# Optimization experiments

Measured on AMD Instinct MI355X. Metric: run time of the kernel, lower is better.

Reference implementation:

```python
import jax, jax.numpy as jnp
import numpy as np

N_NODES = 100000
N_EDGES = 3200000
IN_CH = 128
HID = 64
OUT_CH = 40


def setup_inputs() -> dict:
    key = jax.random.key(0)
    ks = jax.random.split(key, 12)
    x = jax.random.normal(ks[0], (N_NODES, IN_CH), dtype=jnp.float32)
    edge_index = jax.random.randint(ks[1], (2, N_EDGES), 0, N_NODES, dtype=jnp.int64)
    def lin(k, fan_in, fan_out):
        bound = 1.0 / np.sqrt(fan_in)
        kw, kb = jax.random.split(k)
        W = jax.random.uniform(kw, (fan_in, fan_out), minval=-bound, maxval=bound, dtype=jnp.float32)
        b = jax.random.uniform(kb, (fan_out,), minval=-bound, maxval=bound, dtype=jnp.float32)
        return W, b
    W1, b1 = lin(ks[2], IN_CH, HID)   # nn1 layer 1
    W2, b2 = lin(ks[3], HID, HID)     # nn1 layer 2
    W3, b3 = lin(ks[4], HID, HID)     # nn2 layer 1
    W4, b4 = lin(ks[5], HID, HID)     # nn2 layer 2
    Wf, bf = lin(ks[6], HID, OUT_CH)  # final fc
    return {"x": x, "edge_index": edge_index,
            "W1": W1, "b1": b1, "W2": W2, "b2": b2,
            "W3": W3, "b3": b3, "W4": W4, "b4": b4,
            "Wf": Wf, "bf": bf}


def _gin_conv(x, src, dst, W_a, b_a, W_b, b_b):
    # GINConv (eps=0): out = MLP(x + sum_{j->i} x_j)
    agg = jax.ops.segment_sum(x[src], dst, num_segments=x.shape[0])
    h = x + agg
    h = jax.nn.relu(h @ W_a + b_a)
    return h @ W_b + b_b


def reference(x, edge_index, W1, b1, W2, b2, W3, b3, W4, b4, Wf, bf):
    src, dst = edge_index[0], edge_index[1]
    h = _gin_conv(x, src, dst, W1, b1, W2, b2)
    h = jax.nn.relu(h)  # dropout is identity at eval
    h = _gin_conv(h, src, dst, W3, b3, W4, b4)
    h = jax.nn.relu(h)
    logits = h @ Wf + bf
    return jax.nn.log_softmax(logits, axis=1)
```

## Files before the change

kernel.cpp:

```cpp
#include <hip/hip_runtime.h>
#include <math.h>

#define N_NODES_C 100000
#define N_EDGES_C 3200000
#define NB 782
#define BNODES 128
#define LDS_CAP 6144
#define CHUNK 8192
#define NBLK 391

typedef unsigned short u16;

__device__ __forceinline__ float bf2f(u16 u) {
    unsigned int t = ((unsigned int)u) << 16;
    return __uint_as_float(t);
}
__device__ __forceinline__ u16 f2bf(float f) {
    unsigned int x = __float_as_uint(f);
    x += 0x7fffu + ((x >> 16) & 1u);
    return (u16)(x >> 16);
}


__global__ __launch_bounds__(256) void passA_hist_kernel(const int* __restrict__ dst,
                                                         int* __restrict__ cnt, int n_edges) {
    __shared__ int h[NB];
    for (int i = threadIdx.x; i < NB; i += 256) h[i] = 0;
    __syncthreads();
    const int blk = blockIdx.x;
    const int e0 = blk * CHUNK;
    const int cntE = min(CHUNK, n_edges - e0);
    for (int i = threadIdx.x * 4; i < cntE; i += 1024) {
        int4 d4 = *(const int4*)&dst[e0 + i];
        atomicAdd(&h[d4.x >> 7], 1); atomicAdd(&h[d4.y >> 7], 1);
        atomicAdd(&h[d4.z >> 7], 1); atomicAdd(&h[d4.w >> 7], 1);
    }
    __syncthreads();
    for (int i = threadIdx.x; i < NB; i += 256) cnt[i * NBLK + blk] = h[i];
}

__global__ __launch_bounds__(256) void scan_chunks_kernel(int* __restrict__ a, int n, int* __restrict__ bsums) {
    __shared__ int s[256];
    const int tid = threadIdx.x;
    int base = blockIdx.x * 1024 + tid * 4;
    int v[4];
#pragma unroll
    for (int i = 0; i < 4; ++i) v[i] = (base + i < n) ? a[base + i] : 0;
    int tsum = v[0] + v[1] + v[2] + v[3];
    s[tid] = tsum;
    __syncthreads();
    for (int off = 1; off < 256; off <<= 1) {
        int t = (tid >= off) ? s[tid - off] : 0;
        __syncthreads();
        s[tid] += t;
        __syncthreads();
    }
    int run = s[tid] - tsum;
#pragma unroll
    for (int i = 0; i < 4; ++i) {
        run += v[i];
        if (base + i < n) a[base + i] = run;
    }
    if (tid == 255) bsums[blockIdx.x] = s[255];
}

__global__ __launch_bounds__(512) void scan_sums_kernel(int* __restrict__ bsums, int nb) {
    __shared__ int s[512];
    const int tid = threadIdx.x;
    int v = (tid < nb) ? bsums[tid] : 0;
    s[tid] = v;
    __syncthreads();
    for (int off = 1; off < 512; off <<= 1) {
        int t = (tid >= off) ? s[tid - off] : 0;
        __syncthreads();
        s[tid] += t;
        __syncthreads();
    }
    if (tid < nb) bsums[tid] = s[tid] - v;
}

__global__ __launch_bounds__(256) void scan_add_kernel(int* __restrict__ a, int n, const int* __restrict__ bsums) {
    int base = blockIdx.x * 1024 + threadIdx.x * 4;
    int add = bsums[blockIdx.x];
#pragma unroll
    for (int i = 0; i < 4; ++i)
        if (base + i < n) a[base + i] += add;
}

__global__ __launch_bounds__(1024) void boffs_kernel(const int* __restrict__ incl,
                                                     int* __restrict__ boffs,
                                                     int* __restrict__ offs) {
    const int b = threadIdx.x;
    if (b < NB) boffs[b] = b ? incl[b * NBLK - 1] : 0;
    if (b == 0) {
        int total = incl[NB * NBLK - 1];
        boffs[NB] = total;
        offs[N_NODES_C] = total;
    }
}

__global__ __launch_bounds__(256) void passB_sort_kernel(const int* __restrict__ src,
                                                         const int* __restrict__ dst,
                                                         const int* __restrict__ incl,
                                                         unsigned int* __restrict__ stage,
                                                         int n_edges) {
    __shared__ unsigned int spack[CHUNK];
    __shared__ int hist[NB];
    __shared__ int lcur[NB];
    __shared__ int tsum[256];
    const int blk = blockIdx.x, tid = threadIdx.x;
    const int e0 = blk * CHUNK;
    const int cntE = min(CHUNK, n_edges - e0);

    for (int b = tid; b < NB; b += 256) hist[b] = 0;
    __syncthreads();

    for (int i = tid * 4; i < cntE; i += 1024) {
        int4 d4 = *(const int4*)&dst[e0 + i];
        atomicAdd(&hist[d4.x >> 7], 1); atomicAdd(&hist[d4.y >> 7], 1);
        atomicAdd(&hist[d4.z >> 7], 1); atomicAdd(&hist[d4.w >> 7], 1);
    }
    __syncthreads();

    {
        int loc[4];
        const int bi = tid * 4;
        int s = 0;
#pragma unroll
        for (int k = 0; k < 4; ++k) {
            int idx = bi + k;
            loc[k] = (idx < NB) ? hist[idx] : 0;
            s += loc[k];
        }
        tsum[tid] = s;
        __syncthreads();
        for (int off = 1; off < 256; off <<= 1) {
            int t = (tid >= off) ? tsum[tid - off] : 0;
            __syncthreads();
            tsum[tid] += t;
            __syncthreads();
        }
        int run = tsum[tid] - s;
#pragma unroll
        for (int k = 0; k < 4; ++k) {
            int idx = bi + k;
            if (idx < NB) {
                int h = loc[k];
                hist[idx] = run;
                lcur[idx] = run;
                run += h;
            }
        }
    }
    __syncthreads();

    for (int i = tid * 4; i < cntE; i += 1024) {
        int4 d4 = *(const int4*)&dst[e0 + i];
        int4 s4 = *(const int4*)&src[e0 + i];
        int p;
        p = atomicAdd(&lcur[d4.x >> 7], 1); spack[p] = (unsigned)s4.x | (((unsigned)d4.x & 127u) << 17);
        p = atomicAdd(&lcur[d4.y >> 7], 1); spack[p] = (unsigned)s4.y | (((unsigned)d4.y & 127u) << 17);
        p = atomicAdd(&lcur[d4.z >> 7], 1); spack[p] = (unsigned)s4.z | (((unsigned)d4.z & 127u) << 17);
        p = atomicAdd(&lcur[d4.w >> 7], 1); spack[p] = (unsigned)s4.w | (((unsigned)d4.w & 127u) << 17);
    }
    __syncthreads();

    for (int b = tid; b < NB; b += 256) {
        int l0 = hist[b];
        int l1 = (b + 1 < NB) ? hist[b + 1] : cntE;
        int idx = b * NBLK + blk;
        int g0 = idx ? incl[idx - 1] : 0;
        for (int j = l0; j < l1; ++j) stage[g0 + (j - l0)] = spack[j];
    }
}

__global__ __launch_bounds__(256) void bucket_finalize_kernel(const unsigned int* __restrict__ stage,
                                                              const int* __restrict__ boffs,
                                                              int* __restrict__ offs,
                                                              int* __restrict__ srcs) {
    __shared__ int hist[BNODES];
    __shared__ int excl[BNODES];
    __shared__ int curs[BNODES];
    __shared__ int sbuf[LDS_CAP];
    const int b = blockIdx.x, tid = threadIdx.x;
    const int base = boffs[b];
    const int count = boffs[b + 1] - base;
    const int n0 = b * BNODES;
    for (int i = tid; i < BNODES; i += 256) hist[i] = 0;
    __syncthreads();
    for (int i = tid; i < count; i += 256) {
        unsigned int w = stage[base + i];
        atomicAdd(&hist[w >> 17], 1);
    }
    __syncthreads();
    if (tid < BNODES) excl[tid] = hist[tid];
    __syncthreads();
    for (int off = 1; off < BNODES; off <<= 1) {
        int t = 0;
        if (tid < BNODES && tid >= off) t = excl[tid - off];
        __syncthreads();
        if (tid < BNODES) excl[tid] += t;
        __syncthreads();
    }
    if (tid < BNODES) {
        int ex = excl[tid] - hist[tid];
        int n = n0 + tid;
        if (n < N_NODES_C) offs[n] = base + ex;
        curs[tid] = ex;
    }
    __syncthreads();
    if (count <= LDS_CAP) {
        for (int i = tid; i < count; i += 256) {
            unsigned int w = stage[base + i];
            int p = atomicAdd(&curs[w >> 17], 1);
            sbuf[p] = (int)(w & 0x1FFFFu);
        }
        __syncthreads();
        for (int i = tid; i < count; i += 256) srcs[base + i] = sbuf[i];
    } else {
        for (int i = tid; i < count; i += 256) {
            unsigned int w = stage[base + i];
            int p = atomicAdd(&curs[w >> 17], 1);
            srcs[base + p] = (int)(w & 0x1FFFFu);
        }
    }
}


__global__ __launch_bounds__(256) void gather64v_kernel(const u16* __restrict__ feat,
                                                        const int* __restrict__ offs,
                                                        const int* __restrict__ srcs,
                                                        const float* __restrict__ bias,
                                                        u16* __restrict__ out, int n_nodes) {
    const int wave = threadIdx.x >> 6;
    const int lane = threadIdx.x & 63;
    const int grp  = lane >> 4;
    const int cl   = lane & 15;
    const int n = blockIdx.x * 4 + wave;
    if (n >= n_nodes) return;

    float a0 = 0.f, a1 = 0.f, a2 = 0.f, a3 = 0.f;
    if (grp == 0) {
        ushort4 v = *(const ushort4*)&feat[(size_t)n * 64 + cl * 4];
        a0 = bf2f(v.x); a1 = bf2f(v.y); a2 = bf2f(v.z); a3 = bf2f(v.w);
    }
    const int s0 = offs[n], s1 = offs[n + 1];
    int i = s0;
    for (; i + 32 <= s1; i += 32) {
        int r[8];
#pragma unroll
        for (int u = 0; u < 8; ++u) r[u] = srcs[i + u * 4 + grp];
        ushort4 v[8];
#pragma unroll
        for (int u = 0; u < 8; ++u) v[u] = *(const ushort4*)&feat[(size_t)r[u] * 64 + cl * 4];
#pragma unroll
        for (int u = 0; u < 8; ++u) {
            a0 += bf2f(v[u].x); a1 += bf2f(v[u].y); a2 += bf2f(v[u].z); a3 += bf2f(v[u].w);
        }
    }
    for (; i + 8 <= s1; i += 8) {
        int ra = srcs[i + grp];
        int rb = srcs[i + 4 + grp];
        ushort4 va = *(const ushort4*)&feat[(size_t)ra * 64 + cl * 4];
        ushort4 vb = *(const ushort4*)&feat[(size_t)rb * 64 + cl * 4];
        a0 += bf2f(va.x); a1 += bf2f(va.y); a2 += bf2f(va.z); a3 += bf2f(va.w);
        a0 += bf2f(vb.x); a1 += bf2f(vb.y); a2 += bf2f(vb.z); a3 += bf2f(vb.w);
    }
    for (; i + 4 <= s1; i += 4) {
        int rr = srcs[i + grp];
        ushort4 v = *(const ushort4*)&feat[(size_t)rr * 64 + cl * 4];
        a0 += bf2f(v.x); a1 += bf2f(v.y); a2 += bf2f(v.z); a3 += bf2f(v.w);
    }
    if (i + grp < s1) {
        int rr = srcs[i + grp];
        ushort4 v = *(const ushort4*)&feat[(size_t)rr * 64 + cl * 4];
        a0 += bf2f(v.x); a1 += bf2f(v.y); a2 += bf2f(v.z); a3 += bf2f(v.w);
    }
    a0 += __shfl_xor(a0, 16); a1 += __shfl_xor(a1, 16);
    a2 += __shfl_xor(a2, 16); a3 += __shfl_xor(a3, 16);
    a0 += __shfl_xor(a0, 32); a1 += __shfl_xor(a1, 32);
    a2 += __shfl_xor(a2, 32); a3 += __shfl_xor(a3, 32);
    if (lane < 16) {
        float4 b = *(const float4*)&bias[cl * 4];
        ushort4 o;
        o.x = f2bf(fmaxf(a0 + b.x, 0.f));
        o.y = f2bf(fmaxf(a1 + b.y, 0.f));
        o.z = f2bf(fmaxf(a2 + b.z, 0.f));
        o.w = f2bf(fmaxf(a3 + b.w, 0.f));
        *(ushort4*)&out[(size_t)n * 64 + cl * 4] = o;
    }
}

#define GIN_STEP(ai, i)                                                                               \
    acc[i][0] += ai.x * w0.x; acc[i][1] += ai.x * w0.y; acc[i][2] += ai.x * w0.z; acc[i][3] += ai.x * w0.w; \
    acc[i][0] += ai.y * w1.x; acc[i][1] += ai.y * w1.y; acc[i][2] += ai.y * w1.z; acc[i][3] += ai.y * w1.w; \
    acc[i][0] += ai.z * w2.x; acc[i][1] += ai.z * w2.y; acc[i][2] += ai.z * w2.z; acc[i][3] += ai.z * w2.w; \
    acc[i][0] += ai.w * w3.x; acc[i][1] += ai.w * w3.y; acc[i][2] += ai.w * w3.z; acc[i][3] += ai.w * w3.w;

#define BF4_TO_F4(u4) make_float4(bf2f(u4.x), bf2f(u4.y), bf2f(u4.z), bf2f(u4.w))


__global__ __launch_bounds__(256) void dense128_kernel(const float* __restrict__ in,
                                                       const float* __restrict__ W,
                                                       u16* __restrict__ out, int n_nodes) {
    __shared__ float sW[128 * 64];
    const int tid = threadIdx.x;
    for (int i = tid; i < 128 * 16; i += 256) ((float4*)sW)[i] = ((const float4*)W)[i];
    __syncthreads();
    const int tj = tid & 15, tn = tid >> 4;
    const int j0 = tj * 4, n0 = blockIdx.x * 64 + tn * 4;
    const int r0 = min(n0 + 0, n_nodes - 1), r1 = min(n0 + 1, n_nodes - 1);
    const int r2 = min(n0 + 2, n_nodes - 1), r3 = min(n0 + 3, n_nodes - 1);
    float acc[4][4];
#pragma unroll
    for (int i = 0; i < 4; ++i)
#pragma unroll
        for (int j = 0; j < 4; ++j) acc[i][j] = 0.f;
#pragma unroll 4
    for (int k = 0; k < 128; k += 4) {
        float4 a0 = *(const float4*)&in[(size_t)r0 * 128 + k];
        float4 a1 = *(const float4*)&in[(size_t)r1 * 128 + k];
        float4 a2 = *(const float4*)&in[(size_t)r2 * 128 + k];
        float4 a3 = *(const float4*)&in[(size_t)r3 * 128 + k];
        float4 w0 = *(const float4*)&sW[(k + 0) * 64 + j0];
        float4 w1 = *(const float4*)&sW[(k + 1) * 64 + j0];
        float4 w2 = *(const float4*)&sW[(k + 2) * 64 + j0];
        float4 w3 = *(const float4*)&sW[(k + 3) * 64 + j0];
        GIN_STEP(a0, 0) GIN_STEP(a1, 1) GIN_STEP(a2, 2) GIN_STEP(a3, 3)
    }
#pragma unroll
    for (int i = 0; i < 4; ++i) {
        int n = n0 + i;
        if (n < n_nodes) {
            ushort4 o;
            o.x = f2bf(acc[i][0]); o.y = f2bf(acc[i][1]);
            o.z = f2bf(acc[i][2]); o.w = f2bf(acc[i][3]);
            *(ushort4*)&out[(size_t)n * 64 + j0] = o;
        }
    }
}


__global__ __launch_bounds__(256) void fused_w2w3_kernel(const u16* __restrict__ in,
                                                         const float* __restrict__ W2,
                                                         const float* __restrict__ b2,
                                                         const float* __restrict__ W3,
                                                         u16* __restrict__ out, int n_nodes) {
    __shared__ float sW2[64 * 64];
    __shared__ float sW3[64 * 64];
    __shared__ float sT[64][68];
    const int tid = threadIdx.x;
    for (int i = tid; i < 64 * 16; i += 256) {
        ((float4*)sW2)[i] = ((const float4*)W2)[i];
        ((float4*)sW3)[i] = ((const float4*)W3)[i];
    }
    __syncthreads();
    const int tj = tid & 15, tn = tid >> 4;
    const int j0 = tj * 4, n0l = tn * 4;
    const int base = blockIdx.x * 64;
    const int r0 = min(base + n0l + 0, n_nodes - 1), r1 = min(base + n0l + 1, n_nodes - 1);
    const int r2 = min(base + n0l + 2, n_nodes - 1), r3 = min(base + n0l + 3, n_nodes - 1);
    float acc[4][4];
#pragma unroll
    for (int i = 0; i < 4; ++i)
#pragma unroll
        for (int j = 0; j < 4; ++j) acc[i][j] = b2[j0 + j];
#pragma unroll 4
    for (int k = 0; k < 64; k += 4) {
        ushort4 u0 = *(const ushort4*)&in[(size_t)r0 * 64 + k];
        ushort4 u1 = *(const ushort4*)&in[(size_t)r1 * 64 + k];
        ushort4 u2 = *(const ushort4*)&in[(size_t)r2 * 64 + k];
        ushort4 u3 = *(const ushort4*)&in[(size_t)r3 * 64 + k];
        float4 a0 = BF4_TO_F4(u0);
        float4 a1 = BF4_TO_F4(u1);
        float4 a2 = BF4_TO_F4(u2);
        float4 a3 = BF4_TO_F4(u3);
        float4 w0 = *(const float4*)&sW2[(k + 0) * 64 + j0];
        float4 w1 = *(const float4*)&sW2[(k + 1) * 64 + j0];
        float4 w2 = *(const float4*)&sW2[(k + 2) * 64 + j0];
        float4 w3 = *(const float4*)&sW2[(k + 3) * 64 + j0];
        GIN_STEP(a0, 0) GIN_STEP(a1, 1) GIN_STEP(a2, 2) GIN_STEP(a3, 3)
    }
#pragma unroll
    for (int i = 0; i < 4; ++i) {
        float4 t;
        t.x = fmaxf(acc[i][0], 0.f); t.y = fmaxf(acc[i][1], 0.f);
        t.z = fmaxf(acc[i][2], 0.f); t.w = fmaxf(acc[i][3], 0.f);
        *(float4*)&sT[n0l + i][j0] = t;
    }
    __syncthreads();
#pragma unroll
    for (int i = 0; i < 4; ++i)
#pragma unroll
        for (int j = 0; j < 4; ++j) acc[i][j] = 0.f;
#pragma unroll 4
    for (int k = 0; k < 64; k += 4) {
        float4 a0 = *(const float4*)&sT[n0l + 0][k];
        float4 a1 = *(const float4*)&sT[n0l + 1][k];
        float4 a2 = *(const float4*)&sT[n0l + 2][k];
        float4 a3 = *(const float4*)&sT[n0l + 3][k];
        float4 w0 = *(const float4*)&sW3[(k + 0) * 64 + j0];
        float4 w1 = *(const float4*)&sW3[(k + 1) * 64 + j0];
        float4 w2 = *(const float4*)&sW3[(k + 2) * 64 + j0];
        float4 w3 = *(const float4*)&sW3[(k + 3) * 64 + j0];
        GIN_STEP(a0, 0) GIN_STEP(a1, 1) GIN_STEP(a2, 2) GIN_STEP(a3, 3)
    }
#pragma unroll
    for (int i = 0; i < 4; ++i) {
        int n = base + n0l + i;
        if (n < n_nodes) {
            ushort4 o;
            o.x = f2bf(acc[i][0]); o.y = f2bf(acc[i][1]);
            o.z = f2bf(acc[i][2]); o.w = f2bf(acc[i][3]);
            *(ushort4*)&out[(size_t)n * 64 + j0] = o;
        }
    }
}


__global__ __launch_bounds__(256) void fused_w4final_kernel(const u16* __restrict__ in,
                                                            const float* __restrict__ W4,
                                                            const float* __restrict__ b4,
                                                            const float* __restrict__ Wf,
                                                            const float* __restrict__ bfin,
                                                            float* __restrict__ out, int n_nodes) {
    __shared__ float smem[11008];
    float* sW4 = smem;
    float* sWf = smem + 4096;
    float* sTf = smem + 6656;
    float* sLog = smem;
    const int tid = threadIdx.x;
    const int base = blockIdx.x * 64;
    for (int i = tid; i < 64 * 16; i += 256) ((float4*)sW4)[i] = ((const float4*)W4)[i];
    for (int i = tid; i < 64 * 10; i += 256) ((float4*)sWf)[i] = ((const float4*)Wf)[i];
    __syncthreads();
    {
        const int tj = tid & 15, tn = tid >> 4;
        const int j0 = tj * 4, n0l = tn * 4;
        const int r0 = min(base + n0l + 0, n_nodes - 1), r1 = min(base + n0l + 1, n_nodes - 1);
        const int r2 = min(base + n0l + 2, n_nodes - 1), r3 = min(base + n0l + 3, n_nodes - 1);
        float acc[4][4];
#pragma unroll
        for (int i = 0; i < 4; ++i)
#pragma unroll
            for (int j = 0; j < 4; ++j) acc[i][j] = b4[j0 + j];
#pragma unroll 4
        for (int k = 0; k < 64; k += 4) {
            ushort4 u0 = *(const ushort4*)&in[(size_t)r0 * 64 + k];
            ushort4 u1 = *(const ushort4*)&in[(size_t)r1 * 64 + k];
            ushort4 u2 = *(const ushort4*)&in[(size_t)r2 * 64 + k];
            ushort4 u3 = *(const ushort4*)&in[(size_t)r3 * 64 + k];
            float4 a0 = BF4_TO_F4(u0);
            float4 a1 = BF4_TO_F4(u1);
            float4 a2 = BF4_TO_F4(u2);
            float4 a3 = BF4_TO_F4(u3);
            float4 w0 = *(const float4*)&sW4[(k + 0) * 64 + j0];
            float4 w1 = *(const float4*)&sW4[(k + 1) * 64 + j0];
            float4 w2 = *(const float4*)&sW4[(k + 2) * 64 + j0];
            float4 w3 = *(const float4*)&sW4[(k + 3) * 64 + j0];
            GIN_STEP(a0, 0) GIN_STEP(a1, 1) GIN_STEP(a2, 2) GIN_STEP(a3, 3)
        }
#pragma unroll
        for (int i = 0; i < 4; ++i) {
            float4 t;
            t.x = fmaxf(acc[i][0], 0.f); t.y = fmaxf(acc[i][1], 0.f);
            t.z = fmaxf(acc[i][2], 0.f); t.w = fmaxf(acc[i][3], 0.f);
            *(float4*)&sTf[(n0l + i) * 68 + j0] = t;
        }
    }
    __syncthreads();
    if (tid < 160) {
        const int tj = tid % 10, tn = tid / 10;
        const int j0 = tj * 4, n0l = tn * 4;
        float acc[4][4];
#pragma unroll
        for (int i = 0; i < 4; ++i)
#pragma unroll
            for (int j = 0; j < 4; ++j) acc[i][j] = bfin[j0 + j];
#pragma unroll 4
        for (int k = 0; k < 64; k += 4) {
            float4 a0 = *(const float4*)&sTf[(n0l + 0) * 68 + k];
            float4 a1 = *(const float4*)&sTf[(n0l + 1) * 68 + k];
            float4 a2 = *(const float4*)&sTf[(n0l + 2) * 68 + k];
            float4 a3 = *(const float4*)&sTf[(n0l + 3) * 68 + k];
            float4 w0 = *(const float4*)&sWf[(k + 0) * 40 + j0];
            float4 w1 = *(const float4*)&sWf[(k + 1) * 40 + j0];
            float4 w2 = *(const float4*)&sWf[(k + 2) * 40 + j0];
            float4 w3 = *(const float4*)&sWf[(k + 3) * 40 + j0];
            GIN_STEP(a0, 0) GIN_STEP(a1, 1) GIN_STEP(a2, 2) GIN_STEP(a3, 3)
        }
#pragma unroll
        for (int i = 0; i < 4; ++i)
            *(float4*)&sLog[(n0l + i) * 40 + j0] = make_float4(acc[i][0], acc[i][1], acc[i][2], acc[i][3]);
    }
    __syncthreads();
    if (tid < 64) {
        const int nl = tid;
        const int n = base + nl;
        if (n < n_nodes) {
            float m = -1e30f;
            for (int j = 0; j < 40; ++j) m = fmaxf(m, sLog[nl * 40 + j]);
            float s = 0.f;
            for (int j = 0; j < 40; ++j) s += expf(sLog[nl * 40 + j] - m);
            float lse = m + logf(s);
            for (int j = 0; j < 40; j += 4) {
                float4 o;
                o.x = sLog[nl * 40 + j + 0] - lse;
                o.y = sLog[nl * 40 + j + 1] - lse;
                o.z = sLog[nl * 40 + j + 2] - lse;
                o.w = sLog[nl * 40 + j + 3] - lse;
                *(float4*)&out[(size_t)n * 40 + j] = o;
            }
        }
    }
}


extern "C" void kernel_launch(void* const* d_in, const int* in_sizes, int n_in,
                              void* d_out, int out_size, void* d_ws, size_t ws_size,
                              hipStream_t stream) {
    const float* x  = (const float*)d_in[0];
    const int*   ei = (const int*)d_in[1];
    const float* W1 = (const float*)d_in[2];
    const float* b1 = (const float*)d_in[3];
    const float* W2 = (const float*)d_in[4];
    const float* b2 = (const float*)d_in[5];
    const float* W3 = (const float*)d_in[6];
    const float* b3 = (const float*)d_in[7];
    const float* W4 = (const float*)d_in[8];
    const float* b4 = (const float*)d_in[9];
    const float* Wf = (const float*)d_in[10];
    const float* bf = (const float*)d_in[11];
    float* outp = (float*)d_out;

    const int N = N_NODES_C, E = N_EDGES_C;
    const int* srcp = ei;
    const int* dstp = ei + E;

    char* ws = (char*)d_ws;
    int*          offs  = (int*)(ws);
    int*          boffs = (int*)(ws + 400128);
    int*          bsums = (int*)(ws + 403328);
    int*          cnt   = (int*)(ws + 405376);
    unsigned int* stage = (unsigned int*)(ws + 1628672);
    int*          srcs  = (int*)(ws + 14428672);
    u16*          Ybf   = (u16*)(ws + 27228672);
    u16*          F2bf  = (u16*)(ws + 40028672);

    passA_hist_kernel<<<NBLK, 256, 0, stream>>>(dstp, cnt, E);
    const int n_scan = NB * NBLK;
    const int nblk_scan = (n_scan + 1023) / 1024;
    scan_chunks_kernel<<<nblk_scan, 256, 0, stream>>>(cnt, n_scan, bsums);
    scan_sums_kernel<<<1, 512, 0, stream>>>(bsums, nblk_scan);
    scan_add_kernel<<<nblk_scan, 256, 0, stream>>>(cnt, n_scan, bsums);
    boffs_kernel<<<1, 1024, 0, stream>>>(cnt, boffs, offs);
    passB_sort_kernel<<<NBLK, 256, 0, stream>>>(srcp, dstp, cnt, stage, E);
    bucket_finalize_kernel<<<NB, 256, 0, stream>>>(stage, boffs, offs, srcs);

    const int mlp_grid = (N + 63) / 64;
    const int gat_grid = (N + 3) / 4;

    dense128_kernel<<<mlp_grid, 256, 0, stream>>>(x, W1, Ybf, N);
    gather64v_kernel<<<gat_grid, 256, 0, stream>>>(Ybf, offs, srcs, b1, F2bf, N);
    fused_w2w3_kernel<<<mlp_grid, 256, 0, stream>>>(F2bf, W2, b2, W3, Ybf, N);

    gather64v_kernel<<<gat_grid, 256, 0, stream>>>(Ybf, offs, srcs, b3, F2bf, N);
    fused_w4final_kernel<<<mlp_grid, 256, 0, stream>>>(F2bf, W4, b4, Wf, bf, outp, N);
}
```

Baseline: 289.1 us.

## Use bf16 MFMA for the fused MLP-layer kernels

Rewrites the two fused dense kernels (W2+W3, and W4+final+log_softmax) to use 16x16x32 bf16 MFMA instructions instead of scalar FP32 FMA loops. Weights are converted to bf16 and pre-arranged in LDS in fragment order, and intermediate activations are kept in LDS as bf16. This is meant to cut the ALU cost of the per-node matmuls, at the price of extra bf16 rounding on the weights and intermediates, plus per-block weight conversion overhead.

```diff
diff --git a/kernel.cpp b/kernel.cpp
--- a/kernel.cpp
+++ b/kernel.cpp
@@ -10,6 +10,8 @@
 #define NBLK 391
 
 typedef unsigned short u16;
+typedef __attribute__((ext_vector_type(8))) short short8v;
+typedef __attribute__((ext_vector_type(4))) float float4v;
 
 __device__ __forceinline__ float bf2f(u16 u) {
     unsigned int t = ((unsigned int)u) << 16;
@@ -297,8 +299,6 @@
     acc[i][0] += ai.z * w2.x; acc[i][1] += ai.z * w2.y; acc[i][2] += ai.z * w2.z; acc[i][3] += ai.z * w2.w; \
     acc[i][0] += ai.w * w3.x; acc[i][1] += ai.w * w3.y; acc[i][2] += ai.w * w3.z; acc[i][3] += ai.w * w3.w;
 
-#define BF4_TO_F4(u4) make_float4(bf2f(u4.x), bf2f(u4.y), bf2f(u4.z), bf2f(u4.w))
-
 
 __global__ __launch_bounds__(256) void dense128_kernel(const float* __restrict__ in,
                                                        const float* __restrict__ W,
@@ -341,162 +341,132 @@
 }
 
 
-__global__ __launch_bounds__(256) void fused_w2w3_kernel(const u16* __restrict__ in,
-                                                         const float* __restrict__ W2,
-                                                         const float* __restrict__ b2,
-                                                         const float* __restrict__ W3,
-                                                         u16* __restrict__ out, int n_nodes) {
-    __shared__ float sW2[64 * 64];
-    __shared__ float sW3[64 * 64];
-    __shared__ float sT[64][68];
+__global__ __launch_bounds__(256) void mfma_w2w3_kernel(const u16* __restrict__ in,
+                                                        const float* __restrict__ W2,
+                                                        const float* __restrict__ b2,
+                                                        const float* __restrict__ W3,
+                                                        u16* __restrict__ out, int n_nodes) {
+    __shared__ u16 w2f[4096];
+    __shared__ u16 w3f[4096];
+    __shared__ u16 sT[64 * 72];
     const int tid = threadIdx.x;
-    for (int i = tid; i < 64 * 16; i += 256) {
-        ((float4*)sW2)[i] = ((const float4*)W2)[i];
-        ((float4*)sW3)[i] = ((const float4*)W3)[i];
-    }
-    __syncthreads();
-    const int tj = tid & 15, tn = tid >> 4;
-    const int j0 = tj * 4, n0l = tn * 4;
-    const int base = blockIdx.x * 64;
-    const int r0 = min(base + n0l + 0, n_nodes - 1), r1 = min(base + n0l + 1, n_nodes - 1);
-    const int r2 = min(base + n0l + 2, n_nodes - 1), r3 = min(base + n0l + 3, n_nodes - 1);
-    float acc[4][4];
-#pragma unroll
-    for (int i = 0; i < 4; ++i)
-#pragma unroll
-        for (int j = 0; j < 4; ++j) acc[i][j] = b2[j0 + j];
-#pragma unroll 4
-    for (int k = 0; k < 64; k += 4) {
-        ushort4 u0 = *(const ushort4*)&in[(size_t)r0 * 64 + k];
-        ushort4 u1 = *(const ushort4*)&in[(size_t)r1 * 64 + k];
-        ushort4 u2 = *(const ushort4*)&in[(size_t)r2 * 64 + k];
-        ushort4 u3 = *(const ushort4*)&in[(size_t)r3 * 64 + k];
-        float4 a0 = BF4_TO_F4(u0);
-        float4 a1 = BF4_TO_F4(u1);
-        float4 a2 = BF4_TO_F4(u2);
-        float4 a3 = BF4_TO_F4(u3);
-        float4 w0 = *(const float4*)&sW2[(k + 0) * 64 + j0];
-        float4 w1 = *(const float4*)&sW2[(k + 1) * 64 + j0];
-        float4 w2 = *(const float4*)&sW2[(k + 2) * 64 + j0];
-        float4 w3 = *(const float4*)&sW2[(k + 3) * 64 + j0];
-        GIN_STEP(a0, 0) GIN_STEP(a1, 1) GIN_STEP(a2, 2) GIN_STEP(a3, 3)
-    }
-#pragma unroll
-    for (int i = 0; i < 4; ++i) {
-        float4 t;
-        t.x = fmaxf(acc[i][0], 0.f); t.y = fmaxf(acc[i][1], 0.f);
-        t.z = fmaxf(acc[i][2], 0.f); t.w = fmaxf(acc[i][3], 0.f);
-        *(float4*)&sT[n0l + i][j0] = t;
-    }
-    __syncthreads();
-#pragma unroll
-    for (int i = 0; i < 4; ++i)
-#pragma unroll
-        for (int j = 0; j < 4; ++j) acc[i][j] = 0.f;
-#pragma unroll 4
-    for (int k = 0; k < 64; k += 4) {
-        float4 a0 = *(const float4*)&sT[n0l + 0][k];
-        float4 a1 = *(const float4*)&sT[n0l + 1][k];
-        float4 a2 = *(const float4*)&sT[n0l + 2][k];
-        float4 a3 = *(const float4*)&sT[n0l + 3][k];
-        float4 w0 = *(const float4*)&sW3[(k + 0) * 64 + j0];
-        float4 w1 = *(const float4*)&sW3[(k + 1) * 64 + j0];
-        float4 w2 = *(const float4*)&sW3[(k + 2) * 64 + j0];
-        float4 w3 = *(const float4*)&sW3[(k + 3) * 64 + j0];
-        GIN_STEP(a0, 0) GIN_STEP(a1, 1) GIN_STEP(a2, 2) GIN_STEP(a3, 3)
-    }
-#pragma unroll
-    for (int i = 0; i < 4; ++i) {
-        int n = base + n0l + i;
-        if (n < n_nodes) {
-            ushort4 o;
-            o.x = f2bf(acc[i][0]); o.y = f2bf(acc[i][1]);
-            o.z = f2bf(acc[i][2]); o.w = f2bf(acc[i][3]);
-            *(ushort4*)&out[(size_t)n * 64 + j0] = o;
-        }
-    }
-}
-
-
-__global__ __launch_bounds__(256) void fused_w4final_kernel(const u16* __restrict__ in,
-                                                            const float* __restrict__ W4,
-                                                            const float* __restrict__ b4,
-                                                            const float* __restrict__ Wf,
-                                                            const float* __restrict__ bfin,
-                                                            float* __restrict__ out, int n_nodes) {
-    __shared__ float smem[11008];
-    float* sW4 = smem;
-    float* sWf = smem + 4096;
-    float* sTf = smem + 6656;
-    float* sLog = smem;
+    for (int idx = tid; idx < 4096; idx += 256) {
+        int frag = idx >> 9;
+        int within = idx & 511;
+        int lane = within >> 3;
+        int i = within & 7;
+        int kt = frag >> 2, jt = frag & 3;
+        int k = kt * 32 + (lane >> 4) * 8 + i;
+        int j = jt * 16 + (lane & 15);
+        w2f[idx] = f2bf(W2[k * 64 + j]);
+        w3f[idx] = f2bf(W3[k * 64 + j]);
+    }
+    __syncthreads();
+    const int w = tid >> 6, l = tid & 63;
+    const int nbase = blockIdx.x * 64 + w * 16;
+    const int arow = min(nbase + (l & 15), n_nodes - 1);
+    short8v a0 = *(const short8v*)&in[(size_t)arow * 64 + (l >> 4) * 8];
+    short8v a1 = *(const short8v*)&in[(size_t)arow * 64 + 32 + (l >> 4) * 8];
+#pragma unroll
+    for (int jt = 0; jt < 4; ++jt) {
+        float bv = b2[jt * 16 + (l & 15)];
+        float4v acc = {bv, bv, bv, bv};
+        acc = __builtin_amdgcn_mfma_f32_16x16x32_bf16(a0, *(short8v*)&w2f[(0 * 4 + jt) * 512 + l * 8], acc, 0, 0, 0);
+        acc = __builtin_amdgcn_mfma_f32_16x16x32_bf16(a1, *(short8v*)&w2f[(1 * 4 + jt) * 512 + l * 8], acc, 0, 0, 0);
+#pragma unroll
+        for (int r = 0; r < 4; ++r) {
+            int row = w * 16 + (l >> 4) * 4 + r;
+            sT[row * 72 + jt * 16 + (l & 15)] = f2bf(fmaxf(acc[r], 0.f));
+        }
+    }
+    __syncthreads();
+    const int trow = w * 16 + (l & 15);
+    short8v t0 = *(short8v*)&sT[trow * 72 + (l >> 4) * 8];
+    short8v t1 = *(short8v*)&sT[trow * 72 + 32 + (l >> 4) * 8];
+#pragma unroll
+    for (int jt = 0; jt < 4; ++jt) {
+        float4v acc = {0.f, 0.f, 0.f, 0.f};
+        acc = __builtin_amdgcn_mfma_f32_16x16x32_bf16(t0, *(short8v*)&w3f[(0 * 4 + jt) * 512 + l * 8], acc, 0, 0, 0);
+        acc = __builtin_amdgcn_mfma_f32_16x16x32_bf16(t1, *(short8v*)&w3f[(1 * 4 + jt) * 512 + l * 8], acc, 0, 0, 0);
+#pragma unroll
+        for (int r = 0; r < 4; ++r) {
+            int n = nbase + (l >> 4) * 4 + r;
+            if (n < n_nodes) out[(size_t)n * 64 + jt * 16 + (l & 15)] = f2bf(acc[r]);
+        }
+    }
+}
+
+
+__global__ __launch_bounds__(256) void mfma_w4final_kernel(const u16* __restrict__ in,
+                                                           const float* __restrict__ W4,
+                                                           const float* __restrict__ b4,
+                                                           const float* __restrict__ Wf,
+                                                           const float* __restrict__ bfin,
+                                                           float* __restrict__ out, int n_nodes) {
+    __shared__ u16 w4f[4096];
+    __shared__ u16 wff[3072];
+    __shared__ u16 sT[64 * 72];
+    __shared__ float sLog[64 * 40];
     const int tid = threadIdx.x;
-    const int base = blockIdx.x * 64;
-    for (int i = tid; i < 64 * 16; i += 256) ((float4*)sW4)[i] = ((const float4*)W4)[i];
-    for (int i = tid; i < 64 * 10; i += 256) ((float4*)sWf)[i] = ((const float4*)Wf)[i];
-    __syncthreads();
-    {
-        const int tj = tid & 15, tn = tid >> 4;
-        const int j0 = tj * 4, n0l = tn * 4;
-        const int r0 = min(base + n0l + 0, n_nodes - 1), r1 = min(base + n0l + 1, n_nodes - 1);
-        const int r2 = min(base + n0l + 2, n_nodes - 1), r3 = min(base + n0l + 3, n_nodes - 1);
-        float acc[4][4];
-#pragma unroll
-        for (int i = 0; i < 4; ++i)
-#pragma unroll
-            for (int j = 0; j < 4; ++j) acc[i][j] = b4[j0 + j];
-#pragma unroll 4
-        for (int k = 0; k < 64; k += 4) {
-            ushort4 u0 = *(const ushort4*)&in[(size_t)r0 * 64 + k];
-            ushort4 u1 = *(const ushort4*)&in[(size_t)r1 * 64 + k];
-            ushort4 u2 = *(const ushort4*)&in[(size_t)r2 * 64 + k];
-            ushort4 u3 = *(const ushort4*)&in[(size_t)r3 * 64 + k];
-            float4 a0 = BF4_TO_F4(u0);
-            float4 a1 = BF4_TO_F4(u1);
-            float4 a2 = BF4_TO_F4(u2);
-            float4 a3 = BF4_TO_F4(u3);
-            float4 w0 = *(const float4*)&sW4[(k + 0) * 64 + j0];
-            float4 w1 = *(const float4*)&sW4[(k + 1) * 64 + j0];
-            float4 w2 = *(const float4*)&sW4[(k + 2) * 64 + j0];
-            float4 w3 = *(const float4*)&sW4[(k + 3) * 64 + j0];
-            GIN_STEP(a0, 0) GIN_STEP(a1, 1) GIN_STEP(a2, 2) GIN_STEP(a3, 3)
-        }
-#pragma unroll
-        for (int i = 0; i < 4; ++i) {
-            float4 t;
-            t.x = fmaxf(acc[i][0], 0.f); t.y = fmaxf(acc[i][1], 0.f);
-            t.z = fmaxf(acc[i][2], 0.f); t.w = fmaxf(acc[i][3], 0.f);
-            *(float4*)&sTf[(n0l + i) * 68 + j0] = t;
-        }
-    }
-    __syncthreads();
-    if (tid < 160) {
-        const int tj = tid % 10, tn = tid / 10;
-        const int j0 = tj * 4, n0l = tn * 4;
-        float acc[4][4];
-#pragma unroll
-        for (int i = 0; i < 4; ++i)
-#pragma unroll
-            for (int j = 0; j < 4; ++j) acc[i][j] = bfin[j0 + j];
-#pragma unroll 4
-        for (int k = 0; k < 64; k += 4) {
-            float4 a0 = *(const float4*)&sTf[(n0l + 0) * 68 + k];
-            float4 a1 = *(const float4*)&sTf[(n0l + 1) * 68 + k];
-            float4 a2 = *(const float4*)&sTf[(n0l + 2) * 68 + k];
-            float4 a3 = *(const float4*)&sTf[(n0l + 3) * 68 + k];
-            float4 w0 = *(const float4*)&sWf[(k + 0) * 40 + j0];
-            float4 w1 = *(const float4*)&sWf[(k + 1) * 40 + j0];
-            float4 w2 = *(const float4*)&sWf[(k + 2) * 40 + j0];
-            float4 w3 = *(const float4*)&sWf[(k + 3) * 40 + j0];
-            GIN_STEP(a0, 0) GIN_STEP(a1, 1) GIN_STEP(a2, 2) GIN_STEP(a3, 3)
-        }
-#pragma unroll
-        for (int i = 0; i < 4; ++i)
-            *(float4*)&sLog[(n0l + i) * 40 + j0] = make_float4(acc[i][0], acc[i][1], acc[i][2], acc[i][3]);
+    for (int idx = tid; idx < 4096; idx += 256) {
+        int frag = idx >> 9;
+        int within = idx & 511;
+        int lane = within >> 3;
+        int i = within & 7;
+        int kt = frag >> 2, jt = frag & 3;
+        int k = kt * 32 + (lane >> 4) * 8 + i;
+        int j = jt * 16 + (lane & 15);
+        w4f[idx] = f2bf(W4[k * 64 + j]);
+    }
+    for (int idx = tid; idx < 3072; idx += 256) {
+        int frag = idx >> 9;
+        int within = idx & 511;
+        int lane = within >> 3;
+        int i = within & 7;
+        int kt = frag / 3, jt = frag % 3;
+        int k = kt * 32 + (lane >> 4) * 8 + i;
+        int j = jt * 16 + (lane & 15);
+        wff[idx] = (j < 40) ? f2bf(Wf[k * 40 + j]) : (u16)0;
+    }
+    __syncthreads();
+    const int w = tid >> 6, l = tid & 63;
+    const int nbase = blockIdx.x * 64 + w * 16;
+    const int arow = min(nbase + (l & 15), n_nodes - 1);
+    short8v a0 = *(const short8v*)&in[(size_t)arow * 64 + (l >> 4) * 8];
+    short8v a1 = *(const short8v*)&in[(size_t)arow * 64 + 32 + (l >> 4) * 8];
+#pragma unroll
+    for (int jt = 0; jt < 4; ++jt) {
+        float bv = b4[jt * 16 + (l & 15)];
+        float4v acc = {bv, bv, bv, bv};
+        acc = __builtin_amdgcn_mfma_f32_16x16x32_bf16(a0, *(short8v*)&w4f[(0 * 4 + jt) * 512 + l * 8], acc, 0, 0, 0);
+        acc = __builtin_amdgcn_mfma_f32_16x16x32_bf16(a1, *(short8v*)&w4f[(1 * 4 + jt) * 512 + l * 8], acc, 0, 0, 0);
+#pragma unroll
+        for (int r = 0; r < 4; ++r) {
+            int row = w * 16 + (l >> 4) * 4 + r;
+            sT[row * 72 + jt * 16 + (l & 15)] = f2bf(fmaxf(acc[r], 0.f));
+        }
+    }
+    __syncthreads();
+    const int trow = w * 16 + (l & 15);
+    short8v t0 = *(short8v*)&sT[trow * 72 + (l >> 4) * 8];
+    short8v t1 = *(short8v*)&sT[trow * 72 + 32 + (l >> 4) * 8];
+#pragma unroll
+    for (int jt = 0; jt < 3; ++jt) {
+        int col = jt * 16 + (l & 15);
+        float bv = (col < 40) ? bfin[col] : 0.f;
+        float4v acc = {bv, bv, bv, bv};
+        acc = __builtin_amdgcn_mfma_f32_16x16x32_bf16(t0, *(short8v*)&wff[(0 * 3 + jt) * 512 + l * 8], acc, 0, 0, 0);
+        acc = __builtin_amdgcn_mfma_f32_16x16x32_bf16(t1, *(short8v*)&wff[(1 * 3 + jt) * 512 + l * 8], acc, 0, 0, 0);
+#pragma unroll
+        for (int r = 0; r < 4; ++r) {
+            int row = w * 16 + (l >> 4) * 4 + r;
+            if (col < 40) sLog[row * 40 + col] = acc[r];
+        }
     }
     __syncthreads();
     if (tid < 64) {
         const int nl = tid;
-        const int n = base + nl;
+        const int n = blockIdx.x * 64 + nl;
         if (n < n_nodes) {
             float m = -1e30f;
             for (int j = 0; j < 40; ++j) m = fmaxf(m, sLog[nl * 40 + j]);
@@ -562,8 +532,8 @@
 
     dense128_kernel<<<mlp_grid, 256, 0, stream>>>(x, W1, Ybf, N);
     gather64v_kernel<<<gat_grid, 256, 0, stream>>>(Ybf, offs, srcs, b1, F2bf, N);
-    fused_w2w3_kernel<<<mlp_grid, 256, 0, stream>>>(F2bf, W2, b2, W3, Ybf, N);
+    mfma_w2w3_kernel<<<mlp_grid, 256, 0, stream>>>(F2bf, W2, b2, W3, Ybf, N);
 
     gather64v_kernel<<<gat_grid, 256, 0, stream>>>(Ybf, offs, srcs, b3, F2bf, N);
-    fused_w4final_kernel<<<mlp_grid, 256, 0, stream>>>(F2bf, W4, b4, Wf, bf, outp, N);
-}
+    mfma_w4final_kernel<<<mlp_grid, 256, 0, stream>>>(F2bf, W4, b4, Wf, bf, outp, N);
+}
```

Measured after the change: 263.7 us. 1.1x faster.
